# Performance work log

Measured on AMD Instinct MI355X. Metric: run time of the kernel, lower is better.

The kernel has to match this reference:

```python
import math
import jax, jax.numpy as jnp
import numpy as np

L, H, K, NH, V, DFF = 6, 512, 512, 8, 64, 1024
B, T, S = 8, 512, 512
PAD = 0


def _ln(x, g, b, eps=1e-5):
    m = jnp.mean(x, -1, keepdims=True)
    v = jnp.mean((x - m) ** 2, -1, keepdims=True)
    return (x - m) * jax.lax.rsqrt(v + eps) * g + b


def _mha(Q, Kin, Vin, mask, wq, bq, wk, bk, wv, bv, wo, bo, g, b):
    # weights stored [in, out]
    B_, Tq, Hd = Q.shape
    dk = wq.shape[1] // NH
    dv = wv.shape[1] // NH
    q = (Q @ wq + bq).reshape(B_, Tq, NH, dk).transpose(0, 2, 1, 3)
    k = (Kin @ wk + bk).reshape(B_, -1, NH, dk).transpose(0, 2, 1, 3)
    v = (Vin @ wv + bv).reshape(B_, -1, NH, dv).transpose(0, 2, 1, 3)
    scores = jnp.einsum('bhqd,bhkd->bhqk', q, k) / jnp.sqrt(jnp.float32(dk))
    scores = jnp.where(mask[:, None, :, :], jnp.float32(-1e9), scores)
    attn = jax.nn.softmax(scores, axis=-1)
    ctx = jnp.einsum('bhqk,bhkd->bhqd', attn, v).transpose(0, 2, 1, 3).reshape(B_, Tq, Hd)
    return _ln(ctx @ wo + bo + Q, g, b)


def _pe(t, d):
    pos = jnp.arange(t, dtype=jnp.float32)[:, None]
    div = jnp.exp(jnp.arange(0, d, 2, dtype=jnp.float32) * (-math.log(10000.0) / d))
    pe = jnp.zeros((t, d), jnp.float32)
    pe = pe.at[:, 0::2].set(jnp.sin(pos * div)).at[:, 1::2].set(jnp.cos(pos * div))
    return pe


def setup_inputs() -> dict:
    key = jax.random.key(0)
    ks = iter(jax.random.split(key, 40))
    nrm = lambda shape, s=0.02: jax.random.normal(next(ks), shape, jnp.float32) * s
    inp = {
        'smiles_index': jax.random.randint(next(ks), (B, T), 0, V, dtype=jnp.int32),
        'enc_outputs': jax.random.normal(next(ks), (B, S, H), jnp.float32),
        'enc_pad_mask': jnp.zeros((B, 1, S), bool),
        'tgt_len': T,
        'mol_emb': nrm((V, H), 1.0).at[PAD].set(0.0),  # padding_idx=0 row zeroed
        # self-attn stacks [L, ...]
        'sa_wq': nrm((L, H, K)), 'sa_bq': jnp.zeros((L, K)),
        'sa_wk': nrm((L, H, K)), 'sa_bk': jnp.zeros((L, K)),
        'sa_wv': nrm((L, H, H)), 'sa_bv': jnp.zeros((L, H)),
        'sa_wo': nrm((L, H, H)), 'sa_bo': jnp.zeros((L, H)),
        'ln1_g': jnp.ones((L, H)), 'ln1_b': jnp.zeros((L, H)),
        # cross-attn stacks
        'ea_wq': nrm((L, H, K)), 'ea_bq': jnp.zeros((L, K)),
        'ea_wk': nrm((L, H, K)), 'ea_bk': jnp.zeros((L, K)),
        'ea_wv': nrm((L, H, H)), 'ea_bv': jnp.zeros((L, H)),
        'ea_wo': nrm((L, H, H)), 'ea_bo': jnp.zeros((L, H)),
        'ln2_g': jnp.ones((L, H)), 'ln2_b': jnp.zeros((L, H)),
        # conv1x1 FFN == per-position linear
        'c1_w': nrm((L, H, DFF)), 'c1_b': jnp.zeros((L, DFF)),
        'c2_w': nrm((L, DFF, H)), 'c2_b': jnp.zeros((L, H)),
        'ln3_g': jnp.ones((L, H)), 'ln3_b': jnp.zeros((L, H)),
    }
    return inp


def reference(smiles_index, enc_outputs, enc_pad_mask, tgt_len, mol_emb,
              sa_wq, sa_bq, sa_wk, sa_bk, sa_wv, sa_bv, sa_wo, sa_bo, ln1_g, ln1_b,
              ea_wq, ea_bq, ea_wk, ea_bk, ea_wv, ea_bv, ea_wo, ea_bo, ln2_g, ln2_b,
              c1_w, c1_b, c2_w, c2_b, ln3_g, ln3_b):
    b, t = smiles_index.shape
    s = enc_outputs.shape[1]
    # embeddings + sinusoidal positional encoding (dropout is identity in eval)
    x = mol_emb[smiles_index] + _pe(t, mol_emb.shape[1])[None]
    # masks: pad (key == pad_id) OR causal upper-triangular
    pad = (smiles_index == PAD)[:, None, :]                 # [B,1,T] -> broadcast over queries
    causal = jnp.triu(jnp.ones((t, t), bool), 1)[None]      # [1,T,T]
    self_mask = pad | causal                                # [B,T,T]
    enc_mask = jnp.broadcast_to(enc_pad_mask, (b, t, s))    # [B,T,S]
    for l in range(L):
        x = _mha(x, x, x, self_mask,
                 sa_wq[l], sa_bq[l], sa_wk[l], sa_bk[l], sa_wv[l], sa_bv[l],
                 sa_wo[l], sa_bo[l], ln1_g[l], ln1_b[l])
        x = _mha(x, enc_outputs, enc_outputs, enc_mask,
                 ea_wq[l], ea_bq[l], ea_wk[l], ea_bk[l], ea_wv[l], ea_bv[l],
                 ea_wo[l], ea_bo[l], ln2_g[l], ln2_b[l])
        h = jax.nn.relu(x @ c1_w[l] + c1_b[l])
        y = h @ c2_w[l] + c2_b[l]
        x = _ln(y + x, ln3_g[l], ln3_b[l])
    return x
```

## Files before the change

kernel.cpp:

```cpp
#include <hip/hip_runtime.h>
#include <hip/hip_bf16.h>
#include <math.h>

#define NL   6
#define HD   512
#define NHD  8
#define DK   64
#define DFFN 1024
#define NB   8
#define TT   512
#define MROWS (NB*TT)

typedef __hip_bfloat16 bf16;
typedef __attribute__((ext_vector_type(8))) short short8v;
typedef __attribute__((ext_vector_type(4))) float f32x4;

__device__ __forceinline__ float wave_sum(float v) {
#pragma unroll
  for (int off = 32; off; off >>= 1) v += __shfl_xor(v, off);
  return v;
}
__device__ __forceinline__ unsigned short f2bf(float x) {
  __hip_bfloat16 h = __float2bfloat16(x);
  return *reinterpret_cast<unsigned short*>(&h);
}

__global__ __launch_bounds__(256)
void wprep_kernel(const float* __restrict__ W, bf16* __restrict__ Wt, int Kd, int Nd) {
  __shared__ float t[32][33];
  const size_t mo = (size_t)blockIdx.z * Kd * Nd;
  const int n0 = blockIdx.x * 32, k0 = blockIdx.y * 32;
  const int tx = threadIdx.x & 31, ty = threadIdx.x >> 5;
#pragma unroll
  for (int j = 0; j < 4; ++j)
    t[ty + j * 8][tx] = W[mo + (size_t)(k0 + ty + j * 8) * Nd + n0 + tx];
  __syncthreads();
#pragma unroll
  for (int j = 0; j < 4; ++j)
    Wt[mo + (size_t)(n0 + ty + j * 8) * Kd + k0 + tx] = __float2bfloat16(t[tx][ty + j * 8]);
}

__global__ __launch_bounds__(256)
void cvtbf16_kernel(const float* __restrict__ in, unsigned short* __restrict__ out) {
  const int i = (blockIdx.x * 256 + threadIdx.x) * 4;
  float4 v = *(const float4*)(in + i);
  out[i + 0] = f2bf(v.x); out[i + 1] = f2bf(v.y);
  out[i + 2] = f2bf(v.z); out[i + 3] = f2bf(v.w);
}

__global__ __launch_bounds__(256)
void embed_pe_kernel(const int* __restrict__ idx, const float* __restrict__ emb,
                     float* __restrict__ x, unsigned short* __restrict__ xb) {
  const int row = blockIdx.x;
  const int t = row & (TT - 1);
  const int tok = idx[row];
  const float cdiv = -0.017988946009466842f;
#pragma unroll
  for (int e0 = 0; e0 < 2; ++e0) {
    const int e = threadIdx.x + e0 * 256;
    const float div = __expf((float)(e & ~1) * cdiv);
    const float ang = (float)t * div;
    const float pe = (e & 1) ? cosf(ang) : sinf(ang);
    const float v = emb[(size_t)tok * HD + e] + pe;
    x[(size_t)row * HD + e] = v;
    xb[(size_t)row * HD + e] = f2bf(v);
  }
}

__device__ __forceinline__ void gemm_compute(const char* As, const char* Bs,
                                             int wm, int wn, int lane,
                                             f32x4 (&acc)[2][2]) {
  const int rsw = (lane & 7) << 4;
  const int csel = (lane >> 4) * 16;
  short8v af[2][2], bfr[2][2];
#pragma unroll
  for (int m = 0; m < 2; ++m)
#pragma unroll
    for (int kk = 0; kk < 2; ++kk) {
      const int row = wm * 32 + m * 16 + (lane & 15);
      af[m][kk] = *(const short8v*)(As + row * 128 + ((kk * 64 + csel) ^ rsw));
    }
#pragma unroll
  for (int n = 0; n < 2; ++n)
#pragma unroll
    for (int kk = 0; kk < 2; ++kk) {
      const int row = wn * 32 + n * 16 + (lane & 15);
      bfr[n][kk] = *(const short8v*)(Bs + row * 128 + ((kk * 64 + csel) ^ rsw));
    }
#pragma unroll
  for (int m = 0; m < 2; ++m)
#pragma unroll
    for (int n = 0; n < 2; ++n) {
      acc[m][n] = __builtin_amdgcn_mfma_f32_16x16x32_bf16(af[m][0], bfr[n][0], acc[m][n], 0, 0, 0);
      acc[m][n] = __builtin_amdgcn_mfma_f32_16x16x32_bf16(af[m][1], bfr[n][1], acc[m][n], 0, 0, 0);
    }
}

template<int OUT_BF16, int RELU>
__global__ __launch_bounds__(256)
void mgemm_kernel(const bf16* __restrict__ A, const bf16* __restrict__ Bt,
                  const float* __restrict__ bias, float* __restrict__ Cf,
                  unsigned short* __restrict__ Cb, int M, int N, int K) {
  __shared__ __attribute__((aligned(16))) char As[64 * 128];
  __shared__ __attribute__((aligned(16))) char Bs[64 * 128];

  const int tid = threadIdx.x;
  const int w = tid >> 6, lane = tid & 63;
  const int wm = w >> 1, wn = w & 1;
  const int m0 = blockIdx.x * 64, n0 = blockIdx.y * 64;

  const int sr = w * 16 + (lane >> 3);
  const int scol = (lane & 7) * 16;
  const int swc = scol ^ ((sr & 7) << 4);
  const bf16* ga0 = A + (size_t)(m0 + sr) * K + (scol >> 1);
  const bf16* ga1 = A + (size_t)(m0 + sr + 8) * K + (scol >> 1);
  const bf16* gb0 = Bt + (size_t)(n0 + sr) * K + (scol >> 1);
  const bf16* gb1 = Bt + (size_t)(n0 + sr + 8) * K + (scol >> 1);
  char* la0 = As + sr * 128 + swc;
  char* la1 = As + (sr + 8) * 128 + swc;
  char* lb0 = Bs + sr * 128 + swc;
  char* lb1 = Bs + (sr + 8) * 128 + swc;

  f32x4 acc[2][2] = {};

  short8v ra0 = *(const short8v*)ga0, ra1 = *(const short8v*)ga1;
  short8v rb0 = *(const short8v*)gb0, rb1 = *(const short8v*)gb1;
  short8v sa0, sa1, sb0, sb1;

  for (int k0 = 0; k0 < K; k0 += 128) {
    __syncthreads();
    *(short8v*)la0 = ra0; *(short8v*)la1 = ra1;
    *(short8v*)lb0 = rb0; *(short8v*)lb1 = rb1;
    __syncthreads();
    sa0 = *(const short8v*)(ga0 + k0 + 64); sa1 = *(const short8v*)(ga1 + k0 + 64);
    sb0 = *(const short8v*)(gb0 + k0 + 64); sb1 = *(const short8v*)(gb1 + k0 + 64);
    gemm_compute(As, Bs, wm, wn, lane, acc);
    __syncthreads();
    *(short8v*)la0 = sa0; *(short8v*)la1 = sa1;
    *(short8v*)lb0 = sb0; *(short8v*)lb1 = sb1;
    __syncthreads();
    if (k0 + 128 < K) {
      ra0 = *(const short8v*)(ga0 + k0 + 128); ra1 = *(const short8v*)(ga1 + k0 + 128);
      rb0 = *(const short8v*)(gb0 + k0 + 128); rb1 = *(const short8v*)(gb1 + k0 + 128);
    }
    gemm_compute(As, Bs, wm, wn, lane, acc);
  }

  const int crow = (lane >> 4) * 4;
  const int ccol = lane & 15;
#pragma unroll
  for (int m = 0; m < 2; ++m)
#pragma unroll
    for (int n = 0; n < 2; ++n) {
      const int gr = m0 + wm * 32 + m * 16 + crow;
      const int gc = n0 + wn * 32 + n * 16 + ccol;
      const float bs = bias[gc];
#pragma unroll
      for (int r = 0; r < 4; ++r) {
        float v = acc[m][n][r] + bs;
        if (RELU) v = fmaxf(v, 0.f);
        if (OUT_BF16) Cb[(size_t)(gr + r) * N + gc] = f2bf(v);
        else          Cf[(size_t)(gr + r) * N + gc] = v;
      }
    }
}

template<int CAUSAL>
__global__ __launch_bounds__(256)
void mattn_kernel(const unsigned short* __restrict__ q, const unsigned short* __restrict__ kgl,
                  const unsigned short* __restrict__ vgl, unsigned short* __restrict__ ctx,
                  const int* __restrict__ idx, const unsigned char* __restrict__ emask) {
  __shared__ __attribute__((aligned(16))) unsigned short kt[64 * 64];
  __shared__ __attribute__((aligned(16))) unsigned short vt[64 * 64];
  __shared__ __attribute__((aligned(16))) unsigned short pl[4][16 * 64];
  __shared__ float km[64];

  const int bh = blockIdx.x;
  const int b = bh >> 3, h = bh & 7;
  const int qbase = blockIdx.y * 64;
  const int tid = threadIdx.x, w = tid >> 6, lane = tid & 63;
  const int l4 = lane & 15, g = lane >> 4;

  const unsigned short* qp = q + (size_t)(b * TT + qbase + w * 16 + l4) * HD + h * DK + g * 8;
  short8v aq0 = *(const short8v*)qp;
  short8v aq1 = *(const short8v*)(qp + 32);

  float m_r[4], l_r[4];
  f32x4 acc_o[4];
#pragma unroll
  for (int r = 0; r < 4; ++r) { m_r[r] = -1e30f; l_r[r] = 0.f; }
#pragma unroll
  for (int f = 0; f < 4; ++f) acc_o[f] = (f32x4){0.f, 0.f, 0.f, 0.f};

  const int kvEnd = CAUSAL ? (qbase + 64) : TT;
  for (int kt0 = 0; kt0 < kvEnd; kt0 += 64) {
    __syncthreads();
    if (tid < 64) {
      const int kp = b * TT + kt0 + tid;
      const bool mk = CAUSAL ? (idx[kp] == 0) : (emask[kp] != 0);
      km[tid] = mk ? 1.f : 0.f;
    }
    {
      const int r = tid >> 2;
      const int bc = (tid & 3) * 32;
      const unsigned short* kp = kgl + (size_t)(b * TT + kt0 + r) * HD + h * DK + (bc >> 1);
      short8v ka = *(const short8v*)kp;
      short8v kb2 = *(const short8v*)(kp + 8);
      const int sw = (r & 7) << 4;
      *(short8v*)((char*)kt + r * 128 + (bc ^ sw)) = ka;
      *(short8v*)((char*)kt + r * 128 + ((bc + 16) ^ sw)) = kb2;
    }
    {
      const int k2 = (tid & 31) * 2;
      const int d0 = (tid >> 5) * 8;
      const unsigned short* vp0 = vgl + (size_t)(b * TT + kt0 + k2) * HD + h * DK + d0;
      const unsigned short* vp1 = vp0 + HD;
      short8v v0 = *(const short8v*)vp0;
      short8v v1 = *(const short8v*)vp1;
#pragma unroll
      for (int j = 0; j < 8; ++j) {
        const int d = d0 + j;
        const unsigned pk = ((unsigned)(unsigned short)v0[j]) | (((unsigned)(unsigned short)v1[j]) << 16);
        *(unsigned*)((char*)vt + d * 128 + ((k2 * 2) ^ ((d & 7) << 4))) = pk;
      }
    }
    __syncthreads();

    f32x4 s4[4];
#pragma unroll
    for (int f = 0; f < 4; ++f) {
      const int krow = f * 16 + l4;
      const int sw = (krow & 7) << 4;
      short8v bk0 = *(const short8v*)((const char*)kt + krow * 128 + ((g * 16) ^ sw));
      short8v bk1 = *(const short8v*)((const char*)kt + krow * 128 + ((64 + g * 16) ^ sw));
      f32x4 a = {};
      a = __builtin_amdgcn_mfma_f32_16x16x32_bf16(aq0, bk0, a, 0, 0, 0);
      a = __builtin_amdgcn_mfma_f32_16x16x32_bf16(aq1, bk1, a, 0, 0, 0);
      s4[f] = a;
    }

    float sc_r[4];
#pragma unroll
    for (int r = 0; r < 4; ++r) {
      const int qpos = qbase + w * 16 + g * 4 + r;
      float sf[4];
#pragma unroll
      for (int f = 0; f < 4; ++f) {
        const int kpos = kt0 + f * 16 + l4;
        float s = s4[f][r] * 0.125f;
        const bool msk = (km[f * 16 + l4] != 0.f) || (CAUSAL && kpos > qpos);
        sf[f] = msk ? -1e9f : s;
      }
      float mx = fmaxf(fmaxf(sf[0], sf[1]), fmaxf(sf[2], sf[3]));
#pragma unroll
      for (int off = 8; off; off >>= 1) mx = fmaxf(mx, __shfl_xor(mx, off));
      const float mn = fmaxf(m_r[r], mx);
      const float sc = __expf(m_r[r] - mn);
      m_r[r] = mn;
      sc_r[r] = sc;
      float ps = 0.f;
      const int prow = g * 4 + r;
      const int psw = (prow & 7) << 4;
#pragma unroll
      for (int f = 0; f < 4; ++f) {
        const float p = __expf(sf[f] - mn);
        ps += p;
        *(unsigned short*)((char*)pl[w] + prow * 128 + ((f * 32 + l4 * 2) ^ psw)) = f2bf(p);
      }
#pragma unroll
      for (int off = 8; off; off >>= 1) ps += __shfl_xor(ps, off);
      l_r[r] = l_r[r] * sc + ps;
    }

#pragma unroll
    for (int f = 0; f < 4; ++f)
#pragma unroll
      for (int r = 0; r < 4; ++r) acc_o[f][r] *= sc_r[r];

    const int asw = (l4 & 7) << 4;
    short8v pa0 = *(const short8v*)((const char*)pl[w] + l4 * 128 + ((g * 16) ^ asw));
    short8v pa1 = *(const short8v*)((const char*)pl[w] + l4 * 128 + ((g * 16 + 64) ^ asw));
#pragma unroll
    for (int f = 0; f < 4; ++f) {
      const int drow = f * 16 + l4;
      const int sw = (drow & 7) << 4;
      short8v vb0 = *(const short8v*)((const char*)vt + drow * 128 + ((g * 16) ^ sw));
      short8v vb1 = *(const short8v*)((const char*)vt + drow * 128 + ((g * 16 + 64) ^ sw));
      acc_o[f] = __builtin_amdgcn_mfma_f32_16x16x32_bf16(pa0, vb0, acc_o[f], 0, 0, 0);
      acc_o[f] = __builtin_amdgcn_mfma_f32_16x16x32_bf16(pa1, vb1, acc_o[f], 0, 0, 0);
    }
  }

  float rl[4];
#pragma unroll
  for (int r = 0; r < 4; ++r) rl[r] = 1.f / l_r[r];
#pragma unroll
  for (int f = 0; f < 4; ++f)
#pragma unroll
    for (int r = 0; r < 4; ++r) {
      const int row = qbase + w * 16 + g * 4 + r;
      const int col = h * DK + f * 16 + l4;
      ctx[(size_t)(b * TT + row) * HD + col] = f2bf(acc_o[f][r] * rl[r]);
    }
}

__global__ __launch_bounds__(256)
void ln_kernel(const float* __restrict__ y, const float* __restrict__ res,
               float* __restrict__ out, unsigned short* __restrict__ outb,
               const float* __restrict__ g, const float* __restrict__ bta) {
  const int row = blockIdx.x;
  const int tid = threadIdx.x;
  const int w = tid >> 6, lane = tid & 63;
  const float* yr = y + (size_t)row * HD;
  const float* rr = res + (size_t)row * HD;

  float v0 = yr[tid] + rr[tid];
  float v1 = yr[tid + 256] + rr[tid + 256];

  __shared__ float red[4];
  float s = wave_sum(v0 + v1);
  if (lane == 0) red[w] = s;
  __syncthreads();
  const float mean = (red[0] + red[1] + red[2] + red[3]) * (1.f / HD);
  __syncthreads();

  const float d0 = v0 - mean, d1 = v1 - mean;
  float qv = wave_sum(d0 * d0 + d1 * d1);
  if (lane == 0) red[w] = qv;
  __syncthreads();
  const float var = (red[0] + red[1] + red[2] + red[3]) * (1.f / HD);
  const float rstd = rsqrtf(var + 1e-5f);

  const float o0 = d0 * rstd * g[tid] + bta[tid];
  const float o1 = d1 * rstd * g[tid + 256] + bta[tid + 256];
  out[(size_t)row * HD + tid] = o0;
  out[(size_t)row * HD + tid + 256] = o1;
  outb[(size_t)row * HD + tid] = f2bf(o0);
  outb[(size_t)row * HD + tid + 256] = f2bf(o1);
}

extern "C" void kernel_launch(void* const* d_in, const int* in_sizes, int n_in,
                              void* d_out, int out_size, void* d_ws, size_t ws_size,
                              hipStream_t stream) {
  const int* idx = (const int*)d_in[0];
  const float* enc = (const float*)d_in[1];
  const unsigned char* emask = (const unsigned char*)d_in[2];
  const float* emb = (const float*)d_in[4];
  const float* sa_wq = (const float*)d_in[5];
  const float* sa_bq = (const float*)d_in[6];
  const float* sa_wk = (const float*)d_in[7];
  const float* sa_bk = (const float*)d_in[8];
  const float* sa_wv = (const float*)d_in[9];
  const float* sa_bv = (const float*)d_in[10];
  const float* sa_wo = (const float*)d_in[11];
  const float* sa_bo = (const float*)d_in[12];
  const float* ln1g = (const float*)d_in[13];
  const float* ln1b = (const float*)d_in[14];
  const float* ea_wq = (const float*)d_in[15];
  const float* ea_bq = (const float*)d_in[16];
  const float* ea_wk = (const float*)d_in[17];
  const float* ea_bk = (const float*)d_in[18];
  const float* ea_wv = (const float*)d_in[19];
  const float* ea_bv = (const float*)d_in[20];
  const float* ea_wo = (const float*)d_in[21];
  const float* ea_bo = (const float*)d_in[22];
  const float* ln2g = (const float*)d_in[23];
  const float* ln2b = (const float*)d_in[24];
  const float* c1w = (const float*)d_in[25];
  const float* c1b = (const float*)d_in[26];
  const float* c2w = (const float*)d_in[27];
  const float* c2b = (const float*)d_in[28];
  const float* ln3g = (const float*)d_in[29];
  const float* ln3b = (const float*)d_in[30];

  const size_t MH = (size_t)MROWS * HD;
  const size_t SQ = (size_t)HD * HD;
  char* ws = (char*)d_ws;
  float*          x    = (float*)(ws + 0);
  unsigned short* xb   = (unsigned short*)(ws + (8u << 20));
  unsigned short* qb   = (unsigned short*)(ws + (12u << 20));
  unsigned short* kb   = (unsigned short*)(ws + (16u << 20));
  unsigned short* vb   = (unsigned short*)(ws + (20u << 20));
  float*          yb   = (float*)(ws + (24u << 20));
  unsigned short* cxb  = (unsigned short*)(ws + (32u << 20));
  unsigned short* encb = (unsigned short*)(ws + (36u << 20));
  bf16*           wt   = (bf16*)(ws + (40u << 20));
  unsigned short* hb   = qb;

  bf16* t_sa_q = wt;
  bf16* t_sa_k = wt + 6 * SQ;
  bf16* t_sa_v = wt + 12 * SQ;
  bf16* t_sa_o = wt + 18 * SQ;
  bf16* t_ea_q = wt + 24 * SQ;
  bf16* t_ea_k = wt + 30 * SQ;
  bf16* t_ea_v = wt + 36 * SQ;
  bf16* t_ea_o = wt + 42 * SQ;
  bf16* t_c1   = wt + 48 * SQ;
  bf16* t_c2   = wt + 48 * SQ + 12 * SQ;

  const dim3 blk(256);
  const dim3 g512(MROWS / 64, HD / 64);
  const dim3 gFF(MROWS / 64, DFFN / 64);
  const dim3 attng(NB * NHD, TT / 64);

  wprep_kernel<<<dim3(16, 16, NL), blk, 0, stream>>>(sa_wq, t_sa_q, HD, HD);
  wprep_kernel<<<dim3(16, 16, NL), blk, 0, stream>>>(sa_wk, t_sa_k, HD, HD);
  wprep_kernel<<<dim3(16, 16, NL), blk, 0, stream>>>(sa_wv, t_sa_v, HD, HD);
  wprep_kernel<<<dim3(16, 16, NL), blk, 0, stream>>>(sa_wo, t_sa_o, HD, HD);
  wprep_kernel<<<dim3(16, 16, NL), blk, 0, stream>>>(ea_wq, t_ea_q, HD, HD);
  wprep_kernel<<<dim3(16, 16, NL), blk, 0, stream>>>(ea_wk, t_ea_k, HD, HD);
  wprep_kernel<<<dim3(16, 16, NL), blk, 0, stream>>>(ea_wv, t_ea_v, HD, HD);
  wprep_kernel<<<dim3(16, 16, NL), blk, 0, stream>>>(ea_wo, t_ea_o, HD, HD);
  wprep_kernel<<<dim3(32, 16, NL), blk, 0, stream>>>(c1w, t_c1, HD, DFFN);
  wprep_kernel<<<dim3(16, 32, NL), blk, 0, stream>>>(c2w, t_c2, DFFN, HD);
  cvtbf16_kernel<<<MH / 1024, blk, 0, stream>>>(enc, encb);

  embed_pe_kernel<<<MROWS, blk, 0, stream>>>(idx, emb, x, xb);

  for (int l = 0; l < NL; ++l) {
    const size_t wo = (size_t)l * SQ;
    const size_t b512 = (size_t)l * HD;
    const size_t w1 = (size_t)l * HD * DFFN;
    const size_t bFF = (size_t)l * DFFN;

    mgemm_kernel<1, 0><<<g512, blk, 0, stream>>>((const bf16*)xb, t_sa_q + wo, sa_bq + b512, nullptr, qb, MROWS, HD, HD);
    mgemm_kernel<1, 0><<<g512, blk, 0, stream>>>((const bf16*)xb, t_sa_k + wo, sa_bk + b512, nullptr, kb, MROWS, HD, HD);
    mgemm_kernel<1, 0><<<g512, blk, 0, stream>>>((const bf16*)xb, t_sa_v + wo, sa_bv + b512, nullptr, vb, MROWS, HD, HD);
    mattn_kernel<1><<<attng, blk, 0, stream>>>(qb, kb, vb, cxb, idx, emask);
    mgemm_kernel<0, 0><<<g512, blk, 0, stream>>>((const bf16*)cxb, t_sa_o + wo, sa_bo + b512, yb, nullptr, MROWS, HD, HD);
    ln_kernel<<<MROWS, blk, 0, stream>>>(yb, x, x, xb, ln1g + b512, ln1b + b512);

    mgemm_kernel<1, 0><<<g512, blk, 0, stream>>>((const bf16*)xb, t_ea_q + wo, ea_bq + b512, nullptr, qb, MROWS, HD, HD);
    mgemm_kernel<1, 0><<<g512, blk, 0, stream>>>((const bf16*)encb, t_ea_k + wo, ea_bk + b512, nullptr, kb, MROWS, HD, HD);
    mgemm_kernel<1, 0><<<g512, blk, 0, stream>>>((const bf16*)encb, t_ea_v + wo, ea_bv + b512, nullptr, vb, MROWS, HD, HD);
    mattn_kernel<0><<<attng, blk, 0, stream>>>(qb, kb, vb, cxb, idx, emask);
    mgemm_kernel<0, 0><<<g512, blk, 0, stream>>>((const bf16*)cxb, t_ea_o + wo, ea_bo + b512, yb, nullptr, MROWS, HD, HD);
    ln_kernel<<<MROWS, blk, 0, stream>>>(yb, x, x, xb, ln2g + b512, ln2b + b512);

    mgemm_kernel<1, 1><<<gFF, blk, 0, stream>>>((const bf16*)xb, t_c1 + w1, c1b + bFF, nullptr, hb, MROWS, DFFN, HD);
    mgemm_kernel<0, 0><<<g512, blk, 0, stream>>>((const bf16*)hb, t_c2 + w1, c2b + b512, yb, nullptr, MROWS, HD, DFFN);
    ln_kernel<<<MROWS, blk, 0, stream>>>(yb, x, x, xb, ln3g + b512, ln3b + b512);
  }

  hipMemcpyAsync(d_out, x, MH * sizeof(float), hipMemcpyDeviceToDevice, stream);
}
```

Measured before the change: 926.8 us.

## Fuse QKV and cross-attn KV projections, widen attention blocks with causal tile skipping

Packs the Q/K/V weights into one concatenated slab (and cross-attn K/V into another), with concatenated biases, so each layer issues one wide GEMM instead of three or two. The attention kernel now uses 512-thread blocks covering 128 queries, so each K/V tile load is shared by twice as many queries. It also skips fully masked causal tiles per wave and only applies the causal compare on diagonal tiles. The mask becomes an additive bias and MFMA sections get raised priority. This trades fewer launches and better operand reuse for strided Q/K/V reads and fewer attention blocks in flight.

```diff
diff --git a/kernel.cpp b/kernel.cpp
--- a/kernel.cpp
+++ b/kernel.cpp
@@ -13,6 +13,7 @@
 
 typedef __hip_bfloat16 bf16;
 typedef __attribute__((ext_vector_type(8))) short short8v;
+typedef __attribute__((ext_vector_type(4))) short short4v;
 typedef __attribute__((ext_vector_type(4))) float f32x4;
 
 __device__ __forceinline__ float wave_sum(float v) {
@@ -26,18 +27,33 @@
 }
 
 __global__ __launch_bounds__(256)
-void wprep_kernel(const float* __restrict__ W, bf16* __restrict__ Wt, int Kd, int Nd) {
+void wprep_kernel(const float* __restrict__ W, bf16* __restrict__ Wt, int Kd, int Nd,
+                  int dstRowOff, int dstSlabRows) {
   __shared__ float t[32][33];
-  const size_t mo = (size_t)blockIdx.z * Kd * Nd;
+  const size_t src = (size_t)blockIdx.z * Kd * Nd;
+  const size_t dst = (size_t)blockIdx.z * dstSlabRows * Kd;
   const int n0 = blockIdx.x * 32, k0 = blockIdx.y * 32;
   const int tx = threadIdx.x & 31, ty = threadIdx.x >> 5;
 #pragma unroll
   for (int j = 0; j < 4; ++j)
-    t[ty + j * 8][tx] = W[mo + (size_t)(k0 + ty + j * 8) * Nd + n0 + tx];
+    t[ty + j * 8][tx] = W[src + (size_t)(k0 + ty + j * 8) * Nd + n0 + tx];
   __syncthreads();
 #pragma unroll
   for (int j = 0; j < 4; ++j)
-    Wt[mo + (size_t)(n0 + ty + j * 8) * Kd + k0 + tx] = __float2bfloat16(t[tx][ty + j * 8]);
+    Wt[dst + (size_t)(dstRowOff + n0 + ty + j * 8) * Kd + k0 + tx] =
+        __float2bfloat16(t[tx][ty + j * 8]);
+}
+
+__global__ __launch_bounds__(256)
+void bcat_kernel(const float* __restrict__ b0, const float* __restrict__ b1,
+                 const float* __restrict__ b2, float* __restrict__ out, int nseg) {
+  const int l = blockIdx.x;
+  const int stride = 512 * nseg;
+  for (int i = threadIdx.x; i < stride; i += 256) {
+    const int seg = i >> 9, off = i & 511;
+    const float* src = seg == 0 ? b0 : (seg == 1 ? b1 : b2);
+    out[(size_t)l * stride + i] = src[(size_t)l * 512 + off];
+  }
 }
 
 __global__ __launch_bounds__(256)
@@ -166,22 +182,23 @@
 }
 
 template<int CAUSAL>
-__global__ __launch_bounds__(256)
+__global__ __launch_bounds__(512)
 void mattn_kernel(const unsigned short* __restrict__ q, const unsigned short* __restrict__ kgl,
                   const unsigned short* __restrict__ vgl, unsigned short* __restrict__ ctx,
-                  const int* __restrict__ idx, const unsigned char* __restrict__ emask) {
+                  const int* __restrict__ idx, const unsigned char* __restrict__ emask,
+                  int qstride, int kvstride) {
   __shared__ __attribute__((aligned(16))) unsigned short kt[64 * 64];
   __shared__ __attribute__((aligned(16))) unsigned short vt[64 * 64];
-  __shared__ __attribute__((aligned(16))) unsigned short pl[4][16 * 64];
+  __shared__ __attribute__((aligned(16))) unsigned short pl[8][16 * 64];
   __shared__ float km[64];
 
   const int bh = blockIdx.x;
   const int b = bh >> 3, h = bh & 7;
-  const int qbase = blockIdx.y * 64;
+  const int qbase = blockIdx.y * 128;
   const int tid = threadIdx.x, w = tid >> 6, lane = tid & 63;
   const int l4 = lane & 15, g = lane >> 4;
 
-  const unsigned short* qp = q + (size_t)(b * TT + qbase + w * 16 + l4) * HD + h * DK + g * 8;
+  const unsigned short* qp = q + (size_t)(b * TT + qbase + w * 16 + l4) * qstride + h * DK + g * 8;
   short8v aq0 = *(const short8v*)qp;
   short8v aq1 = *(const short8v*)(qp + 32);
 
@@ -192,102 +209,112 @@
 #pragma unroll
   for (int f = 0; f < 4; ++f) acc_o[f] = (f32x4){0.f, 0.f, 0.f, 0.f};
 
-  const int kvEnd = CAUSAL ? (qbase + 64) : TT;
+  const int kvEnd = CAUSAL ? (qbase + 128) : TT;
   for (int kt0 = 0; kt0 < kvEnd; kt0 += 64) {
     __syncthreads();
     if (tid < 64) {
       const int kp = b * TT + kt0 + tid;
       const bool mk = CAUSAL ? (idx[kp] == 0) : (emask[kp] != 0);
-      km[tid] = mk ? 1.f : 0.f;
+      km[tid] = mk ? -1e9f : 0.f;
     }
     {
-      const int r = tid >> 2;
-      const int bc = (tid & 3) * 32;
-      const unsigned short* kp = kgl + (size_t)(b * TT + kt0 + r) * HD + h * DK + (bc >> 1);
-      short8v ka = *(const short8v*)kp;
-      short8v kb2 = *(const short8v*)(kp + 8);
-      const int sw = (r & 7) << 4;
-      *(short8v*)((char*)kt + r * 128 + (bc ^ sw)) = ka;
-      *(short8v*)((char*)kt + r * 128 + ((bc + 16) ^ sw)) = kb2;
+      const int r = tid >> 3, c8 = tid & 7;
+      const unsigned short* kp = kgl + (size_t)(b * TT + kt0 + r) * kvstride + h * DK + c8 * 8;
+      short8v kv = *(const short8v*)kp;
+      *(short8v*)((char*)kt + r * 128 + ((c8 * 16) ^ ((r & 7) << 4))) = kv;
     }
     {
       const int k2 = (tid & 31) * 2;
-      const int d0 = (tid >> 5) * 8;
-      const unsigned short* vp0 = vgl + (size_t)(b * TT + kt0 + k2) * HD + h * DK + d0;
-      const unsigned short* vp1 = vp0 + HD;
-      short8v v0 = *(const short8v*)vp0;
-      short8v v1 = *(const short8v*)vp1;
-#pragma unroll
-      for (int j = 0; j < 8; ++j) {
-        const int d = d0 + j;
+      const int d4 = (tid >> 5) * 4;
+      const unsigned short* vp0 = vgl + (size_t)(b * TT + kt0 + k2) * kvstride + h * DK + d4;
+      const unsigned short* vp1 = vp0 + kvstride;
+      short4v v0 = *(const short4v*)vp0;
+      short4v v1 = *(const short4v*)vp1;
+#pragma unroll
+      for (int j = 0; j < 4; ++j) {
+        const int d = d4 + j;
         const unsigned pk = ((unsigned)(unsigned short)v0[j]) | (((unsigned)(unsigned short)v1[j]) << 16);
         *(unsigned*)((char*)vt + d * 128 + ((k2 * 2) ^ ((d & 7) << 4))) = pk;
       }
     }
     __syncthreads();
 
-    f32x4 s4[4];
-#pragma unroll
-    for (int f = 0; f < 4; ++f) {
-      const int krow = f * 16 + l4;
-      const int sw = (krow & 7) << 4;
-      short8v bk0 = *(const short8v*)((const char*)kt + krow * 128 + ((g * 16) ^ sw));
-      short8v bk1 = *(const short8v*)((const char*)kt + krow * 128 + ((64 + g * 16) ^ sw));
-      f32x4 a = {};
-      a = __builtin_amdgcn_mfma_f32_16x16x32_bf16(aq0, bk0, a, 0, 0, 0);
-      a = __builtin_amdgcn_mfma_f32_16x16x32_bf16(aq1, bk1, a, 0, 0, 0);
-      s4[f] = a;
-    }
-
-    float sc_r[4];
-#pragma unroll
-    for (int r = 0; r < 4; ++r) {
-      const int qpos = qbase + w * 16 + g * 4 + r;
-      float sf[4];
+    if (!(CAUSAL && kt0 > qbase + w * 16 + 15)) {
+      const bool diag = CAUSAL && (kt0 + 64 > qbase + w * 16);
+
+      f32x4 s4[4];
+      __builtin_amdgcn_s_setprio(1);
 #pragma unroll
       for (int f = 0; f < 4; ++f) {
-        const int kpos = kt0 + f * 16 + l4;
-        float s = s4[f][r] * 0.125f;
-        const bool msk = (km[f * 16 + l4] != 0.f) || (CAUSAL && kpos > qpos);
-        sf[f] = msk ? -1e9f : s;
+        const int krow = f * 16 + l4;
+        const int sw = (krow & 7) << 4;
+        short8v bk0 = *(const short8v*)((const char*)kt + krow * 128 + ((g * 16) ^ sw));
+        short8v bk1 = *(const short8v*)((const char*)kt + krow * 128 + ((64 + g * 16) ^ sw));
+        f32x4 a = {};
+        a = __builtin_amdgcn_mfma_f32_16x16x32_bf16(aq0, bk0, a, 0, 0, 0);
+        a = __builtin_amdgcn_mfma_f32_16x16x32_bf16(aq1, bk1, a, 0, 0, 0);
+        s4[f] = a;
       }
-      float mx = fmaxf(fmaxf(sf[0], sf[1]), fmaxf(sf[2], sf[3]));
-#pragma unroll
-      for (int off = 8; off; off >>= 1) mx = fmaxf(mx, __shfl_xor(mx, off));
-      const float mn = fmaxf(m_r[r], mx);
-      const float sc = __expf(m_r[r] - mn);
-      m_r[r] = mn;
-      sc_r[r] = sc;
-      float ps = 0.f;
-      const int prow = g * 4 + r;
-      const int psw = (prow & 7) << 4;
+      __builtin_amdgcn_s_setprio(0);
+
+      float kmb[4];
+#pragma unroll
+      for (int f = 0; f < 4; ++f) kmb[f] = km[f * 16 + l4];
+
+      float sc_r[4];
+#pragma unroll
+      for (int r = 0; r < 4; ++r) {
+        const int qpos = qbase + w * 16 + g * 4 + r;
+        float sf[4];
+#pragma unroll
+        for (int f = 0; f < 4; ++f) sf[f] = fmaf(s4[f][r], 0.125f, kmb[f]);
+        if (diag) {
+#pragma unroll
+          for (int f = 0; f < 4; ++f) {
+            const int kpos = kt0 + f * 16 + l4;
+            sf[f] = (kpos > qpos) ? -1e9f : sf[f];
+          }
+        }
+        float mx = fmaxf(fmaxf(sf[0], sf[1]), fmaxf(sf[2], sf[3]));
+#pragma unroll
+        for (int off = 8; off; off >>= 1) mx = fmaxf(mx, __shfl_xor(mx, off));
+        const float mn = fmaxf(m_r[r], mx);
+        const float sc = __expf(m_r[r] - mn);
+        m_r[r] = mn;
+        sc_r[r] = sc;
+        float ps = 0.f;
+        const int prow = g * 4 + r;
+        const int psw = (prow & 7) << 4;
+#pragma unroll
+        for (int f = 0; f < 4; ++f) {
+          const float p = __expf(sf[f] - mn);
+          ps += p;
+          *(unsigned short*)((char*)pl[w] + prow * 128 + ((f * 32 + l4 * 2) ^ psw)) = f2bf(p);
+        }
+#pragma unroll
+        for (int off = 8; off; off >>= 1) ps += __shfl_xor(ps, off);
+        l_r[r] = l_r[r] * sc + ps;
+      }
+
+#pragma unroll
+      for (int f = 0; f < 4; ++f)
+#pragma unroll
+        for (int r = 0; r < 4; ++r) acc_o[f][r] *= sc_r[r];
+
+      const int asw = (l4 & 7) << 4;
+      short8v pa0 = *(const short8v*)((const char*)pl[w] + l4 * 128 + ((g * 16) ^ asw));
+      short8v pa1 = *(const short8v*)((const char*)pl[w] + l4 * 128 + ((g * 16 + 64) ^ asw));
+      __builtin_amdgcn_s_setprio(1);
 #pragma unroll
       for (int f = 0; f < 4; ++f) {
-        const float p = __expf(sf[f] - mn);
-        ps += p;
-        *(unsigned short*)((char*)pl[w] + prow * 128 + ((f * 32 + l4 * 2) ^ psw)) = f2bf(p);
+        const int drow = f * 16 + l4;
+        const int sw = (drow & 7) << 4;
+        short8v vb0 = *(const short8v*)((const char*)vt + drow * 128 + ((g * 16) ^ sw));
+        short8v vb1 = *(const short8v*)((const char*)vt + drow * 128 + ((g * 16 + 64) ^ sw));
+        acc_o[f] = __builtin_amdgcn_mfma_f32_16x16x32_bf16(pa0, vb0, acc_o[f], 0, 0, 0);
+        acc_o[f] = __builtin_amdgcn_mfma_f32_16x16x32_bf16(pa1, vb1, acc_o[f], 0, 0, 0);
       }
-#pragma unroll
-      for (int off = 8; off; off >>= 1) ps += __shfl_xor(ps, off);
-      l_r[r] = l_r[r] * sc + ps;
-    }
-
-#pragma unroll
-    for (int f = 0; f < 4; ++f)
-#pragma unroll
-      for (int r = 0; r < 4; ++r) acc_o[f][r] *= sc_r[r];
-
-    const int asw = (l4 & 7) << 4;
-    short8v pa0 = *(const short8v*)((const char*)pl[w] + l4 * 128 + ((g * 16) ^ asw));
-    short8v pa1 = *(const short8v*)((const char*)pl[w] + l4 * 128 + ((g * 16 + 64) ^ asw));
-#pragma unroll
-    for (int f = 0; f < 4; ++f) {
-      const int drow = f * 16 + l4;
-      const int sw = (drow & 7) << 4;
-      short8v vb0 = *(const short8v*)((const char*)vt + drow * 128 + ((g * 16) ^ sw));
-      short8v vb1 = *(const short8v*)((const char*)vt + drow * 128 + ((g * 16 + 64) ^ sw));
-      acc_o[f] = __builtin_amdgcn_mfma_f32_16x16x32_bf16(pa0, vb0, acc_o[f], 0, 0, 0);
-      acc_o[f] = __builtin_amdgcn_mfma_f32_16x16x32_bf16(pa1, vb1, acc_o[f], 0, 0, 0);
+      __builtin_amdgcn_s_setprio(0);
     }
   }
 
@@ -378,67 +405,76 @@
   char* ws = (char*)d_ws;
   float*          x    = (float*)(ws + 0);
   unsigned short* xb   = (unsigned short*)(ws + (8u << 20));
-  unsigned short* qb   = (unsigned short*)(ws + (12u << 20));
-  unsigned short* kb   = (unsigned short*)(ws + (16u << 20));
-  unsigned short* vb   = (unsigned short*)(ws + (20u << 20));
-  float*          yb   = (float*)(ws + (24u << 20));
-  unsigned short* cxb  = (unsigned short*)(ws + (32u << 20));
-  unsigned short* encb = (unsigned short*)(ws + (36u << 20));
-  bf16*           wt   = (bf16*)(ws + (40u << 20));
-  unsigned short* hb   = qb;
-
-  bf16* t_sa_q = wt;
-  bf16* t_sa_k = wt + 6 * SQ;
-  bf16* t_sa_v = wt + 12 * SQ;
-  bf16* t_sa_o = wt + 18 * SQ;
-  bf16* t_ea_q = wt + 24 * SQ;
-  bf16* t_ea_k = wt + 30 * SQ;
-  bf16* t_ea_v = wt + 36 * SQ;
-  bf16* t_ea_o = wt + 42 * SQ;
-  bf16* t_c1   = wt + 48 * SQ;
-  bf16* t_c2   = wt + 48 * SQ + 12 * SQ;
+  unsigned short* qkvb = (unsigned short*)(ws + (12u << 20));
+  unsigned short* qcb  = (unsigned short*)(ws + (24u << 20));
+  unsigned short* kvb  = (unsigned short*)(ws + (28u << 20));
+  unsigned short* cxb  = (unsigned short*)(ws + (36u << 20));
+  float*          yb   = (float*)(ws + (40u << 20));
+  unsigned short* encb = (unsigned short*)(ws + (56u << 20));
+  bf16*           wt   = (bf16*)(ws + (60u << 20));
+  float*          bcS  = (float*)(ws + (98u << 20));
+  float*          bcKV = (float*)(ws + (99u << 20));
+  unsigned short* hb   = qkvb;
+
+  bf16* t_saqkv = wt;
+  bf16* t_sao   = wt + 18 * SQ;
+  bf16* t_eaq   = wt + 24 * SQ;
+  bf16* t_eakv  = wt + 30 * SQ;
+  bf16* t_eao   = wt + 42 * SQ;
+  bf16* t_c1    = wt + 48 * SQ;
+  bf16* t_c2    = wt + 60 * SQ;
 
   const dim3 blk(256);
-  const dim3 g512(MROWS / 64, HD / 64);
-  const dim3 gFF(MROWS / 64, DFFN / 64);
-  const dim3 attng(NB * NHD, TT / 64);
-
-  wprep_kernel<<<dim3(16, 16, NL), blk, 0, stream>>>(sa_wq, t_sa_q, HD, HD);
-  wprep_kernel<<<dim3(16, 16, NL), blk, 0, stream>>>(sa_wk, t_sa_k, HD, HD);
-  wprep_kernel<<<dim3(16, 16, NL), blk, 0, stream>>>(sa_wv, t_sa_v, HD, HD);
-  wprep_kernel<<<dim3(16, 16, NL), blk, 0, stream>>>(sa_wo, t_sa_o, HD, HD);
-  wprep_kernel<<<dim3(16, 16, NL), blk, 0, stream>>>(ea_wq, t_ea_q, HD, HD);
-  wprep_kernel<<<dim3(16, 16, NL), blk, 0, stream>>>(ea_wk, t_ea_k, HD, HD);
-  wprep_kernel<<<dim3(16, 16, NL), blk, 0, stream>>>(ea_wv, t_ea_v, HD, HD);
-  wprep_kernel<<<dim3(16, 16, NL), blk, 0, stream>>>(ea_wo, t_ea_o, HD, HD);
-  wprep_kernel<<<dim3(32, 16, NL), blk, 0, stream>>>(c1w, t_c1, HD, DFFN);
-  wprep_kernel<<<dim3(16, 32, NL), blk, 0, stream>>>(c2w, t_c2, DFFN, HD);
+  const dim3 blk512(512);
+  const dim3 gQKV(MROWS / 64, 1536 / 64);
+  const dim3 g1024(MROWS / 64, 1024 / 64);
+  const dim3 g512(MROWS / 64, 512 / 64);
+  const dim3 attng(NB * NHD, TT / 128);
+
+  wprep_kernel<<<dim3(16, 16, NL), blk, 0, stream>>>(sa_wq, t_saqkv, HD, HD, 0, 1536);
+  wprep_kernel<<<dim3(16, 16, NL), blk, 0, stream>>>(sa_wk, t_saqkv, HD, HD, 512, 1536);
+  wprep_kernel<<<dim3(16, 16, NL), blk, 0, stream>>>(sa_wv, t_saqkv, HD, HD, 1024, 1536);
+  wprep_kernel<<<dim3(16, 16, NL), blk, 0, stream>>>(sa_wo, t_sao, HD, HD, 0, 512);
+  wprep_kernel<<<dim3(16, 16, NL), blk, 0, stream>>>(ea_wq, t_eaq, HD, HD, 0, 512);
+  wprep_kernel<<<dim3(16, 16, NL), blk, 0, stream>>>(ea_wk, t_eakv, HD, HD, 0, 1024);
+  wprep_kernel<<<dim3(16, 16, NL), blk, 0, stream>>>(ea_wv, t_eakv, HD, HD, 512, 1024);
+  wprep_kernel<<<dim3(16, 16, NL), blk, 0, stream>>>(ea_wo, t_eao, HD, HD, 0, 512);
+  wprep_kernel<<<dim3(32, 16, NL), blk, 0, stream>>>(c1w, t_c1, HD, DFFN, 0, 1024);
+  wprep_kernel<<<dim3(16, 32, NL), blk, 0, stream>>>(c2w, t_c2, DFFN, HD, 0, 512);
+  bcat_kernel<<<NL, blk, 0, stream>>>(sa_bq, sa_bk, sa_bv, bcS, 3);
+  bcat_kernel<<<NL, blk, 0, stream>>>(ea_bk, ea_bv, nullptr, bcKV, 2);
   cvtbf16_kernel<<<MH / 1024, blk, 0, stream>>>(enc, encb);
 
   embed_pe_kernel<<<MROWS, blk, 0, stream>>>(idx, emb, x, xb);
 
   for (int l = 0; l < NL; ++l) {
-    const size_t wo = (size_t)l * SQ;
     const size_t b512 = (size_t)l * HD;
-    const size_t w1 = (size_t)l * HD * DFFN;
     const size_t bFF = (size_t)l * DFFN;
 
-    mgemm_kernel<1, 0><<<g512, blk, 0, stream>>>((const bf16*)xb, t_sa_q + wo, sa_bq + b512, nullptr, qb, MROWS, HD, HD);
-    mgemm_kernel<1, 0><<<g512, blk, 0, stream>>>((const bf16*)xb, t_sa_k + wo, sa_bk + b512, nullptr, kb, MROWS, HD, HD);
-    mgemm_kernel<1, 0><<<g512, blk, 0, stream>>>((const bf16*)xb, t_sa_v + wo, sa_bv + b512, nullptr, vb, MROWS, HD, HD);
-    mattn_kernel<1><<<attng, blk, 0, stream>>>(qb, kb, vb, cxb, idx, emask);
-    mgemm_kernel<0, 0><<<g512, blk, 0, stream>>>((const bf16*)cxb, t_sa_o + wo, sa_bo + b512, yb, nullptr, MROWS, HD, HD);
+    mgemm_kernel<1, 0><<<gQKV, blk, 0, stream>>>(
+        (const bf16*)xb, t_saqkv + (size_t)l * 3 * SQ, bcS + (size_t)l * 1536,
+        nullptr, qkvb, MROWS, 1536, HD);
+    mattn_kernel<1><<<attng, blk512, 0, stream>>>(qkvb, qkvb + 512, qkvb + 1024, cxb,
+                                                  idx, emask, 1536, 1536);
+    mgemm_kernel<0, 0><<<g512, blk, 0, stream>>>(
+        (const bf16*)cxb, t_sao + (size_t)l * SQ, sa_bo + b512, yb, nullptr, MROWS, HD, HD);
     ln_kernel<<<MROWS, blk, 0, stream>>>(yb, x, x, xb, ln1g + b512, ln1b + b512);
 
-    mgemm_kernel<1, 0><<<g512, blk, 0, stream>>>((const bf16*)xb, t_ea_q + wo, ea_bq + b512, nullptr, qb, MROWS, HD, HD);
-    mgemm_kernel<1, 0><<<g512, blk, 0, stream>>>((const bf16*)encb, t_ea_k + wo, ea_bk + b512, nullptr, kb, MROWS, HD, HD);
-    mgemm_kernel<1, 0><<<g512, blk, 0, stream>>>((const bf16*)encb, t_ea_v + wo, ea_bv + b512, nullptr, vb, MROWS, HD, HD);
-    mattn_kernel<0><<<attng, blk, 0, stream>>>(qb, kb, vb, cxb, idx, emask);
-    mgemm_kernel<0, 0><<<g512, blk, 0, stream>>>((const bf16*)cxb, t_ea_o + wo, ea_bo + b512, yb, nullptr, MROWS, HD, HD);
+    mgemm_kernel<1, 0><<<g512, blk, 0, stream>>>(
+        (const bf16*)xb, t_eaq + (size_t)l * SQ, ea_bq + b512, nullptr, qcb, MROWS, HD, HD);
+    mgemm_kernel<1, 0><<<g1024, blk, 0, stream>>>(
+        (const bf16*)encb, t_eakv + (size_t)l * 2 * SQ, bcKV + (size_t)l * 1024,
+        nullptr, kvb, MROWS, 1024, HD);
+    mattn_kernel<0><<<attng, blk512, 0, stream>>>(qcb, kvb, kvb + 512, cxb,
+                                                  idx, emask, 512, 1024);
+    mgemm_kernel<0, 0><<<g512, blk, 0, stream>>>(
+        (const bf16*)cxb, t_eao + (size_t)l * SQ, ea_bo + b512, yb, nullptr, MROWS, HD, HD);
     ln_kernel<<<MROWS, blk, 0, stream>>>(yb, x, x, xb, ln2g + b512, ln2b + b512);
 
-    mgemm_kernel<1, 1><<<gFF, blk, 0, stream>>>((const bf16*)xb, t_c1 + w1, c1b + bFF, nullptr, hb, MROWS, DFFN, HD);
-    mgemm_kernel<0, 0><<<g512, blk, 0, stream>>>((const bf16*)hb, t_c2 + w1, c2b + b512, yb, nullptr, MROWS, HD, DFFN);
+    mgemm_kernel<1, 1><<<g1024, blk, 0, stream>>>(
+        (const bf16*)xb, t_c1 + (size_t)l * 2 * SQ, c1b + bFF, nullptr, hb, MROWS, DFFN, HD);
+    mgemm_kernel<0, 0><<<g512, blk, 0, stream>>>(
+        (const bf16*)hb, t_c2 + (size_t)l * 2 * SQ, c2b + b512, yb, nullptr, MROWS, HD, DFFN);
     ln_kernel<<<MROWS, blk, 0, stream>>>(yb, x, x, xb, ln3g + b512, ln3b + b512);
   }
 
```

After: 874.3 us. 1.06x faster.
